# Kernel optimization log

Hardware: AMD Instinct MI355X
Metric: run time of the kernel (lower is better)

Reference implementation:

```python
import jax, jax.numpy as jnp
import numpy as np

B, N, DIN, DM, NH = 8, 2048, 256, 256, 4
DK = DM // NH


def setup_inputs() -> dict:
    key = jax.random.key(0)
    ks = jax.random.split(key, 8)
    x = jax.random.normal(ks[0], (B, N, DIN), dtype=jnp.float32)
    # contiguous valid ranges per sample (padding on both ends), matching
    # the module's assumption that torch.where(mask)[0][0]/[−1] define a span
    starts = jax.random.randint(ks[1], (B,), 0, N // 8)
    lens = jax.random.randint(ks[2], (B,), N // 2, N - N // 8)
    pos = jnp.arange(N)
    attention_mask = ((pos[None, :] >= starts[:, None])
                      & (pos[None, :] < starts[:, None] + lens[:, None])).astype(jnp.int32)
    s = 0.02
    Wq = jax.random.normal(ks[3], (DIN, DM), jnp.float32) * s
    Wk = jax.random.normal(ks[4], (DIN, DM), jnp.float32) * s
    Wv = jax.random.normal(ks[5], (DIN, DM), jnp.float32) * s
    Wo = jax.random.normal(ks[6], (DM, DM), jnp.float32) * s
    bq = jnp.zeros((DM,), jnp.float32)
    bk = jnp.zeros((DM,), jnp.float32)
    bv = jnp.zeros((DM,), jnp.float32)
    bo = jnp.zeros((DM,), jnp.float32)
    return {"x": x, "attention_mask": attention_mask,
            "Wq": Wq, "bq": bq, "Wk": Wk, "bk": bk,
            "Wv": Wv, "bv": bv, "Wo": Wo, "bo": bo}


def reference(x, attention_mask, Wq, bq, Wk, bk, Wv, bv, Wo, bo):
    b, n, _ = x.shape
    nh, dk = NH, DK
    scale = 1.0 / np.sqrt(dk)
    q = (x @ Wq + bq).reshape(b, n, nh, dk).transpose(0, 2, 1, 3)  # [b,h,n,dk]
    k = (x @ Wk + bk).reshape(b, n, nh, dk).transpose(0, 2, 1, 3)
    v = (x @ Wv + bv).reshape(b, n, nh, dk).transpose(0, 2, 1, 3)
    dist = jnp.einsum('bhid,bhjd->bhij', q, k) * scale  # [b,h,n,n]

    # Vectorized equivalent of the per-sample python-loop mask:
    # start = first True index; end = last True index (torch slice start:end
    # is EXCLUSIVE of the last valid position -- preserved faithfully).
    m = attention_mask.astype(bool)
    pos = jnp.arange(n)
    start = jnp.argmax(m, axis=1)                      # [b]
    end = n - 1 - jnp.argmax(m[:, ::-1], axis=1)       # [b] last True index
    valid = (pos[None, :] >= start[:, None]) & (pos[None, :] < end[:, None])  # [b,n]
    bias = jnp.where(valid[:, :, None] & valid[:, None, :], 0.0, -1e10)       # [b,n,n]

    dist = jax.nn.softmax(dist + bias[:, None, :, :], axis=-1)
    att = jnp.einsum('bhij,bhjd->bhid', dist, v)       # [b,h,n,dk]
    att = att.transpose(0, 2, 1, 3).reshape(b, n, nh * dk)
    return att @ Wo + bo
```

## Files before the change

### kernel.cpp

```cpp
#include <hip/hip_runtime.h>
#include <hip/hip_bf16.h>
#include <math.h>

namespace {
constexpr int Bb  = 8;
constexpr int Nn  = 2048;
constexpr int DIN_ = 256;
constexpr int DM_  = 256;
constexpr int NH_  = 4;
constexpr int DK_  = 64;
constexpr int BH_  = Bb * NH_;
constexpr float SCALE = 0.125f;
}

typedef __attribute__((ext_vector_type(8))) _Float16 half8;
typedef __attribute__((ext_vector_type(2))) __fp16 fp16x2;
typedef __attribute__((ext_vector_type(4))) float f32x4;

static __device__ __forceinline__ unsigned pkrtz_u32(float a, float b) {
    union { fp16x2 h; unsigned u; } u;
    u.h = __builtin_amdgcn_cvt_pkrtz(a, b);
    return u.u;
}

static __device__ __forceinline__ half8 h8_from_u32x4(unsigned w0, unsigned w1,
                                                      unsigned w2, unsigned w3) {
    union { unsigned u[4]; half8 h; } u;
    u.u[0] = w0; u.u[1] = w1; u.u[2] = w2; u.u[3] = w3;
    return u.h;
}

__global__ __launch_bounds__(256) void prep_kernel(
    const int* __restrict__ mask, int* __restrict__ bounds,
    const float* __restrict__ x, _Float16* __restrict__ xh,
    const float* __restrict__ W0, const float* __restrict__ W1,
    const float* __restrict__ W2, const float* __restrict__ W3,
    _Float16* __restrict__ T0, _Float16* __restrict__ T1,
    _Float16* __restrict__ T2, _Float16* __restrict__ T3)
{
    const int bid = blockIdx.x;
    const int tid = threadIdx.x;
    if (bid < 8) {
        const int b = bid;
        __shared__ int smin[256], smax[256];
        int lmin = Nn, lmax = -1;
        for (int i = tid; i < Nn; i += 256) {
            if (mask[b * Nn + i]) {
                if (i < lmin) lmin = i;
                if (i > lmax) lmax = i;
            }
        }
        smin[tid] = lmin; smax[tid] = lmax;
        __syncthreads();
        for (int s = 128; s > 0; s >>= 1) {
            if (tid < s) {
                smin[tid] = min(smin[tid], smin[tid + s]);
                smax[tid] = max(smax[tid], smax[tid + s]);
            }
            __syncthreads();
        }
        if (tid == 0) { bounds[b * 2] = smin[0]; bounds[b * 2 + 1] = smax[0]; }
    } else if (bid < 8 + 2048) {
        const size_t i = ((size_t)(bid - 8) * 256 + tid) * 8;
        float4 v0 = *(const float4*)&x[i];
        float4 v1 = *(const float4*)&x[i + 4];
        _Float16 h[8];
        h[0]=(_Float16)v0.x; h[1]=(_Float16)v0.y; h[2]=(_Float16)v0.z; h[3]=(_Float16)v0.w;
        h[4]=(_Float16)v1.x; h[5]=(_Float16)v1.y; h[6]=(_Float16)v1.z; h[7]=(_Float16)v1.w;
        *(uint4*)&xh[i] = *(const uint4*)h;
    } else {
        const int lin = bid - 2056;
        const int wsel = lin >> 6;
        const float* W; _Float16* T;
        switch (wsel) {
            case 0: W = W0; T = T0; break;
            case 1: W = W1; T = T1; break;
            case 2: W = W2; T = T2; break;
            default: W = W3; T = T3; break;
        }
        const int idx = (lin & 63) * 256 + tid;
        const int n = idx & 255;
        const int k0 = (idx >> 8) << 2;
        _Float16 h4[4];
        #pragma unroll
        for (int j = 0; j < 4; ++j) h4[j] = (_Float16)W[(size_t)(k0 + j) * 256 + n];
        *(uint2*)&T[(size_t)n * 256 + k0] = *(const uint2*)h4;
    }
}

__global__ __launch_bounds__(256) void qkv_mfma(
    const _Float16* __restrict__ xh,
    const _Float16* __restrict__ Wtq, const float* __restrict__ bq,
    const _Float16* __restrict__ Wtk, const float* __restrict__ bk,
    const _Float16* __restrict__ Wtv, const float* __restrict__ bv,
    _Float16* __restrict__ Qh, _Float16* __restrict__ Kh, _Float16* __restrict__ Vt)
{
    const int z = blockIdx.z;
    const _Float16* Wt; const float* bias;
    if (z == 0)      { Wt = Wtq; bias = bq; }
    else if (z == 1) { Wt = Wtk; bias = bk; }
    else             { Wt = Wtv; bias = bv; }

    const int m0 = blockIdx.x * 128;
    const int n0 = blockIdx.y * 64;
    const int tid = threadIdx.x;
    const int w = tid >> 6, lane = tid & 63;
    const int a = lane & 15, g = lane >> 4;
    const int mb = m0 + 32 * w;

    f32x4 d0[4] = {{0,0,0,0},{0,0,0,0},{0,0,0,0},{0,0,0,0}};
    f32x4 d1[4] = {{0,0,0,0},{0,0,0,0},{0,0,0,0},{0,0,0,0}};

    const _Float16* A0 = xh + (size_t)(mb + a) * 256 + 8 * g;
    const _Float16* A1 = xh + (size_t)(mb + 16 + a) * 256 + 8 * g;
    const _Float16* Wr0 = Wt + (size_t)(n0 +  0 + a) * 256 + 8 * g;
    const _Float16* Wr1 = Wt + (size_t)(n0 + 16 + a) * 256 + 8 * g;
    const _Float16* Wr2 = Wt + (size_t)(n0 + 32 + a) * 256 + 8 * g;
    const _Float16* Wr3 = Wt + (size_t)(n0 + 48 + a) * 256 + 8 * g;

    #pragma unroll
    for (int kc = 0; kc < 8; ++kc) {
        const half8 af0 = *(const half8*)(A0 + 32 * kc);
        const half8 af1 = *(const half8*)(A1 + 32 * kc);
        const half8 b0 = *(const half8*)(Wr0 + 32 * kc);
        const half8 b1 = *(const half8*)(Wr1 + 32 * kc);
        const half8 b2 = *(const half8*)(Wr2 + 32 * kc);
        const half8 b3 = *(const half8*)(Wr3 + 32 * kc);
        d0[0] = __builtin_amdgcn_mfma_f32_16x16x32_f16(af0, b0, d0[0], 0,0,0);
        d1[0] = __builtin_amdgcn_mfma_f32_16x16x32_f16(af1, b0, d1[0], 0,0,0);
        d0[1] = __builtin_amdgcn_mfma_f32_16x16x32_f16(af0, b1, d0[1], 0,0,0);
        d1[1] = __builtin_amdgcn_mfma_f32_16x16x32_f16(af1, b1, d1[1], 0,0,0);
        d0[2] = __builtin_amdgcn_mfma_f32_16x16x32_f16(af0, b2, d0[2], 0,0,0);
        d1[2] = __builtin_amdgcn_mfma_f32_16x16x32_f16(af1, b2, d1[2], 0,0,0);
        d0[3] = __builtin_amdgcn_mfma_f32_16x16x32_f16(af0, b3, d0[3], 0,0,0);
        d1[3] = __builtin_amdgcn_mfma_f32_16x16x32_f16(af1, b3, d1[3], 0,0,0);
    }

    #pragma unroll
    for (int t = 0; t < 2; ++t) {
        const int mrow = mb + 16 * t + 4 * g;
        #pragma unroll
        for (int nf = 0; nf < 4; ++nf) {
            const f32x4 dv = t == 0 ? d0[nf] : d1[nf];
            const int n = n0 + 16 * nf + a;
            const float bs = bias[n];
            const int bh = (mrow >> 11) * NH_ + (n >> 6);
            const int dk = n & 63;
            if (z < 2) {
                _Float16* out = z ? Kh : Qh;
                #pragma unroll
                for (int r = 0; r < 4; ++r) {
                    const int tok = (mrow + r) & 2047;
                    out[((size_t)bh * Nn + tok) * DK_ + dk] = (_Float16)(dv[r] + bs);
                }
            } else {
                const int tok = mrow & 2047;
                uint2 pk;
                pk.x = pkrtz_u32(dv[0] + bs, dv[1] + bs);
                pk.y = pkrtz_u32(dv[2] + bs, dv[3] + bs);
                *(uint2*)&Vt[((size_t)bh * DK_ + dk) * Nn + tok] = pk;
            }
        }
    }
}

__global__ __launch_bounds__(256) void colmean_kernel(const _Float16* __restrict__ Vt,
                                                      float* __restrict__ cm) {
    const int bh = blockIdx.x;
    const int t = threadIdx.x;
    const int d = t >> 2, part = t & 3;
    const _Float16* src = Vt + ((size_t)bh * DK_ + d) * Nn + part * 512;
    float s = 0.f;
    for (int i = 0; i < 512; i += 8) {
        half8 v = *(const half8*)(src + i);
        #pragma unroll
        for (int j = 0; j < 8; ++j) s += (float)v[j];
    }
    __shared__ float red[64][4];
    red[d][part] = s;
    __syncthreads();
    if (part == 0)
        cm[bh * DK_ + d] = (red[d][0] + red[d][1] + red[d][2] + red[d][3]) * (1.0f / 2048.0f);
}

__global__ __launch_bounds__(256) void flash_mfma(
    const _Float16* __restrict__ Q, const _Float16* __restrict__ K,
    const _Float16* __restrict__ Vt, const int* __restrict__ bounds,
    _Float16* __restrict__ Oh, float* __restrict__ lw)
{
    const int bid = blockIdx.x;
    const int xcd = bid & 7;
    const int rest = bid >> 3;
    const int qb  = rest & 31;
    const int j   = (rest >> 5) & 3;
    const int s   = rest >> 7;
    const int bh  = j * 8 + xcd;
    const int b  = bh >> 2, h = bh & 3;
    const int q0 = qb * 64;
    const int tid  = threadIdx.x;
    const int w    = tid >> 6;
    const int lane = tid & 63;
    const int a = lane & 15, g = lane >> 4;
    const int start = bounds[2 * b], endv = bounds[2 * b + 1];

    if (q0 + 63 < start || q0 >= endv) return;

    __shared__ __align__(16) _Float16 kfr[2][8][512];
    __shared__ __align__(16) _Float16 vfr[2][8][512];

    const _Float16* Qb = Q  + (size_t)bh * Nn * DK_;
    const _Float16* Kb = K  + (size_t)bh * Nn * DK_;
    const _Float16* Vb = Vt + (size_t)bh * DK_ * Nn;

    const int qrow = q0 + 16 * w + a;
    const half8 qf0 = *(const half8*)&Qb[(size_t)qrow * DK_ + 8 * g];
    const half8 qf1 = *(const half8*)&Qb[(size_t)qrow * DK_ + 32 + 8 * g];

    float l_i = 0.0f;
    f32x4 o0 = {0.f,0.f,0.f,0.f}, o1 = {0.f,0.f,0.f,0.f};
    f32x4 o2 = {0.f,0.f,0.f,0.f}, o3 = {0.f,0.f,0.f,0.f};

#define STAGE(cbuf, kt_) do {                                                        \
        _Pragma("unroll")                                                            \
        for (int ff = 0; ff < 2; ++ff) {                                             \
            const int f  = 2 * w + ff;                                               \
            const int tt = f >> 1, cc = f & 1;                                       \
            const _Float16* ks = &Kb[(size_t)((kt_) + 16 * tt + a) * DK_ + 32 * cc + 8 * g]; \
            __builtin_amdgcn_global_load_lds(                                        \
                (const __attribute__((address_space(1))) void*)ks,                   \
                (__attribute__((address_space(3))) void*)&kfr[cbuf][f][0], 16, 0, 0);\
            const _Float16* vs = &Vb[(size_t)(16 * tt + a) * Nn + (kt_) + 32 * cc + 8 * g]; \
            __builtin_amdgcn_global_load_lds(                                        \
                (const __attribute__((address_space(1))) void*)vs,                   \
                (__attribute__((address_space(3))) void*)&vfr[cbuf][f][0], 16, 0, 0);\
        }                                                                            \
    } while (0)

    const int t0 = start >> 6, t1 = (endv + 63) >> 6;
    const int nt = t1 - t0;
    const int n0t = (nt + 1) >> 1;
    const int ts = (s == 0) ? t0 : t0 + n0t;
    const int te = (s == 0) ? t0 + n0t : t1;

    if (ts < te) {
        const int lo = ts * 64, hiend = te * 64;
        int c = 0;
        STAGE(0, lo);

        for (int kt = lo; kt < hiend; kt += 64) {
            const int nxt = kt + 64;
            if (nxt < hiend) {
                STAGE(c ^ 1, nxt);
                asm volatile("s_waitcnt vmcnt(4)" ::: "memory");
            } else {
                asm volatile("s_waitcnt vmcnt(0)" ::: "memory");
            }
            __builtin_amdgcn_s_barrier();

            const _Float16* kf = &kfr[c][0][0];
            const _Float16* vf = &vfr[c][0][0];

            f32x4 st0 = {0.f,0.f,0.f,0.f}, st1 = {0.f,0.f,0.f,0.f};
            f32x4 st2 = {0.f,0.f,0.f,0.f}, st3 = {0.f,0.f,0.f,0.f};
            st0 = __builtin_amdgcn_mfma_f32_16x16x32_f16(*(const half8*)&kf[0*512 + lane*8], qf0, st0, 0,0,0);
            st0 = __builtin_amdgcn_mfma_f32_16x16x32_f16(*(const half8*)&kf[1*512 + lane*8], qf1, st0, 0,0,0);
            st1 = __builtin_amdgcn_mfma_f32_16x16x32_f16(*(const half8*)&kf[2*512 + lane*8], qf0, st1, 0,0,0);
            st1 = __builtin_amdgcn_mfma_f32_16x16x32_f16(*(const half8*)&kf[3*512 + lane*8], qf1, st1, 0,0,0);
            st2 = __builtin_amdgcn_mfma_f32_16x16x32_f16(*(const half8*)&kf[4*512 + lane*8], qf0, st2, 0,0,0);
            st2 = __builtin_amdgcn_mfma_f32_16x16x32_f16(*(const half8*)&kf[5*512 + lane*8], qf1, st2, 0,0,0);
            st3 = __builtin_amdgcn_mfma_f32_16x16x32_f16(*(const half8*)&kf[6*512 + lane*8], qf0, st3, 0,0,0);
            st3 = __builtin_amdgcn_mfma_f32_16x16x32_f16(*(const half8*)&kf[7*512 + lane*8], qf1, st3, 0,0,0);

            float pv[4][4];
            float rsum = 0.0f;
            const bool edge = (kt < start) || (kt + 64 > endv);
            if (edge) {
                #pragma unroll
                for (int t = 0; t < 4; ++t) {
                    const f32x4 sv = (t == 0) ? st0 : (t == 1) ? st1 : (t == 2) ? st2 : st3;
                    #pragma unroll
                    for (int r = 0; r < 4; ++r) {
                        const int col = kt + 16 * t + 4 * g + r;
                        const bool ok = (col >= start) && (col < endv);
                        const float e = ok ? __expf(sv[r] * SCALE) : 0.0f;
                        pv[t][r] = e;
                        rsum += e;
                    }
                }
            } else {
                #pragma unroll
                for (int t = 0; t < 4; ++t) {
                    const f32x4 sv = (t == 0) ? st0 : (t == 1) ? st1 : (t == 2) ? st2 : st3;
                    #pragma unroll
                    for (int r = 0; r < 4; ++r) {
                        const float e = __expf(sv[r] * SCALE);
                        pv[t][r] = e;
                        rsum += e;
                    }
                }
            }
            rsum += __shfl_xor(rsum, 16, 64);
            rsum += __shfl_xor(rsum, 32, 64);
            l_i += rsum;

            unsigned pk[4][2];
            #pragma unroll
            for (int t = 0; t < 4; ++t) {
                pk[t][0] = pkrtz_u32(pv[t][0], pv[t][1]);
                pk[t][1] = pkrtz_u32(pv[t][2], pv[t][3]);
            }
            const int gsel = g >> 1;
            unsigned aw[2][4];
            #pragma unroll
            for (int cq = 0; cq < 2; ++cq) {
                #pragma unroll
                for (int wd = 0; wd < 4; ++wd) {
                    const int srcLane = a + 16 * (2 * (g & 1) + (wd >> 1));
                    const int lo2 = __shfl((int)pk[2 * cq    ][wd & 1], srcLane, 64);
                    const int hi2 = __shfl((int)pk[2 * cq + 1][wd & 1], srcLane, 64);
                    aw[cq][wd] = (unsigned)(gsel ? hi2 : lo2);
                }
            }
            const half8 pa0 = h8_from_u32x4(aw[0][0], aw[0][1], aw[0][2], aw[0][3]);
            const half8 pa1 = h8_from_u32x4(aw[1][0], aw[1][1], aw[1][2], aw[1][3]);

            o0 = __builtin_amdgcn_mfma_f32_16x16x32_f16(pa0, *(const half8*)&vf[0*512 + lane*8], o0, 0,0,0);
            o0 = __builtin_amdgcn_mfma_f32_16x16x32_f16(pa1, *(const half8*)&vf[1*512 + lane*8], o0, 0,0,0);
            o1 = __builtin_amdgcn_mfma_f32_16x16x32_f16(pa0, *(const half8*)&vf[2*512 + lane*8], o1, 0,0,0);
            o1 = __builtin_amdgcn_mfma_f32_16x16x32_f16(pa1, *(const half8*)&vf[3*512 + lane*8], o1, 0,0,0);
            o2 = __builtin_amdgcn_mfma_f32_16x16x32_f16(pa0, *(const half8*)&vf[4*512 + lane*8], o2, 0,0,0);
            o2 = __builtin_amdgcn_mfma_f32_16x16x32_f16(pa1, *(const half8*)&vf[5*512 + lane*8], o2, 0,0,0);
            o3 = __builtin_amdgcn_mfma_f32_16x16x32_f16(pa0, *(const half8*)&vf[6*512 + lane*8], o3, 0,0,0);
            o3 = __builtin_amdgcn_mfma_f32_16x16x32_f16(pa1, *(const half8*)&vf[7*512 + lane*8], o3, 0,0,0);

            asm volatile("" ::: "memory");
            __builtin_amdgcn_s_barrier();
            c ^= 1;
        }
    }
#undef STAGE

    const size_t half = (size_t)Bb * Nn * DM_;
    _Float16* ob = Oh + (size_t)s * half + ((size_t)b * Nn) * DM_ + h * DK_;
    #pragma unroll
    for (int td = 0; td < 4; ++td) {
        const f32x4 ov = (td == 0) ? o0 : (td == 1) ? o1 : (td == 2) ? o2 : o3;
        #pragma unroll
        for (int r = 0; r < 4; ++r) {
            const int qr = q0 + 16 * w + 4 * g + r;
            ob[(size_t)qr * DM_ + 16 * td + a] = (_Float16)ov[r];
        }
    }
    if (g == 0) {
        const int tok = q0 + 16 * w + a;
        lw[(size_t)s * BH_ * Nn + (size_t)bh * Nn + tok] = l_i;
    }
}

__global__ __launch_bounds__(256) void combine_kernel(
    const _Float16* __restrict__ Oh, const float* __restrict__ lw,
    const int* __restrict__ bounds, const float* __restrict__ cm,
    _Float16* __restrict__ att)
{
    const int b  = blockIdx.y;
    const int q0 = blockIdx.x * 64;
    const int t  = threadIdx.x;
    const int row = q0 + (t >> 2);
    const int h   = t & 3;
    const int c0  = h * 64;
    const int start = bounds[2 * b], endv = bounds[2 * b + 1];
    const bool valid = (row >= start) && (row < endv);

    const size_t half = (size_t)Bb * Nn * DM_;
    const size_t rowoff = ((size_t)b * Nn + row) * DM_ + c0;

    float inv = 0.0f;
    if (valid) {
        const int bh = b * NH_ + h;
        const float l0 = lw[(size_t)bh * Nn + row];
        const float l1 = lw[(size_t)BH_ * Nn + (size_t)bh * Nn + row];
        inv = 1.0f / (l0 + l1);
    }

    #pragma unroll
    for (int jj = 0; jj < 64; jj += 8) {
        _Float16 o[8];
        if (valid) {
            half8 a0 = *(const half8*)&Oh[rowoff + jj];
            half8 a1 = *(const half8*)&Oh[half + rowoff + jj];
            #pragma unroll
            for (int k = 0; k < 8; ++k)
                o[k] = (_Float16)(((float)a0[k] + (float)a1[k]) * inv);
        } else {
            #pragma unroll
            for (int k = 0; k < 8; ++k)
                o[k] = (_Float16)cm[b * DM_ + c0 + jj + k];
        }
        *(uint4*)&att[rowoff + jj] = *(const uint4*)o;
    }
}

__global__ __launch_bounds__(256) void proj_mfma(
    const _Float16* __restrict__ A, const _Float16* __restrict__ Wt,
    const float* __restrict__ bias, float* __restrict__ out)
{
    const int m0 = blockIdx.x * 128;
    const int n0 = blockIdx.y * 64;
    const int tid = threadIdx.x;
    const int w = tid >> 6, lane = tid & 63;
    const int a = lane & 15, g = lane >> 4;
    const int mb = m0 + 32 * w;

    f32x4 d0[4] = {{0,0,0,0},{0,0,0,0},{0,0,0,0},{0,0,0,0}};
    f32x4 d1[4] = {{0,0,0,0},{0,0,0,0},{0,0,0,0},{0,0,0,0}};

    const _Float16* A0 = A + (size_t)(mb + a) * 256 + 8 * g;
    const _Float16* A1 = A + (size_t)(mb + 16 + a) * 256 + 8 * g;
    const _Float16* Wr0 = Wt + (size_t)(n0 +  0 + a) * 256 + 8 * g;
    const _Float16* Wr1 = Wt + (size_t)(n0 + 16 + a) * 256 + 8 * g;
    const _Float16* Wr2 = Wt + (size_t)(n0 + 32 + a) * 256 + 8 * g;
    const _Float16* Wr3 = Wt + (size_t)(n0 + 48 + a) * 256 + 8 * g;

    #pragma unroll
    for (int kc = 0; kc < 8; ++kc) {
        const half8 af0 = *(const half8*)(A0 + 32 * kc);
        const half8 af1 = *(const half8*)(A1 + 32 * kc);
        const half8 b0 = *(const half8*)(Wr0 + 32 * kc);
        const half8 b1 = *(const half8*)(Wr1 + 32 * kc);
        const half8 b2 = *(const half8*)(Wr2 + 32 * kc);
        const half8 b3 = *(const half8*)(Wr3 + 32 * kc);
        d0[0] = __builtin_amdgcn_mfma_f32_16x16x32_f16(af0, b0, d0[0], 0,0,0);
        d1[0] = __builtin_amdgcn_mfma_f32_16x16x32_f16(af1, b0, d1[0], 0,0,0);
        d0[1] = __builtin_amdgcn_mfma_f32_16x16x32_f16(af0, b1, d0[1], 0,0,0);
        d1[1] = __builtin_amdgcn_mfma_f32_16x16x32_f16(af1, b1, d1[1], 0,0,0);
        d0[2] = __builtin_amdgcn_mfma_f32_16x16x32_f16(af0, b2, d0[2], 0,0,0);
        d1[2] = __builtin_amdgcn_mfma_f32_16x16x32_f16(af1, b2, d1[2], 0,0,0);
        d0[3] = __builtin_amdgcn_mfma_f32_16x16x32_f16(af0, b3, d0[3], 0,0,0);
        d1[3] = __builtin_amdgcn_mfma_f32_16x16x32_f16(af1, b3, d1[3], 0,0,0);
    }

    #pragma unroll
    for (int t = 0; t < 2; ++t) {
        const int mrow = mb + 16 * t + 4 * g;
        #pragma unroll
        for (int nf = 0; nf < 4; ++nf) {
            const f32x4 dv = t == 0 ? d0[nf] : d1[nf];
            const int n = n0 + 16 * nf + a;
            const float bs = bias[n];
            #pragma unroll
            for (int r = 0; r < 4; ++r)
                out[(size_t)(mrow + r) * DM_ + n] = dv[r] + bs;
        }
    }
}

extern "C" void kernel_launch(void* const* d_in, const int* in_sizes, int n_in,
                              void* d_out, int out_size, void* d_ws, size_t ws_size,
                              hipStream_t stream)
{
    const float* x    = (const float*)d_in[0];
    const int*   mask = (const int*)d_in[1];
    const float* Wq   = (const float*)d_in[2];
    const float* bq   = (const float*)d_in[3];
    const float* Wk   = (const float*)d_in[4];
    const float* bk   = (const float*)d_in[5];
    const float* Wv   = (const float*)d_in[6];
    const float* bv   = (const float*)d_in[7];
    const float* Wo   = (const float*)d_in[8];
    const float* bo   = (const float*)d_in[9];
    float* out = (float*)d_out;

    char* ws = (char*)d_ws;
    size_t off = 0;
    int* bounds = (int*)ws;                 off += 256;
    float* cmv  = (float*)(ws + off);       off += (size_t)BH_ * DK_ * sizeof(float);
    off = (off + 255) & ~(size_t)255;
    float* lw   = (float*)(ws + off);       off += (size_t)2 * BH_ * Nn * sizeof(float);
    const size_t h16_bytes = (size_t)BH_ * Nn * DK_ * sizeof(_Float16);
    _Float16* xh  = (_Float16*)(ws + off); off += h16_bytes;
    _Float16* Qh  = (_Float16*)(ws + off); off += h16_bytes;
    _Float16* Kh  = (_Float16*)(ws + off); off += h16_bytes;
    _Float16* Vt  = (_Float16*)(ws + off); off += h16_bytes;
    _Float16* Oh  = (_Float16*)(ws + off); off += 2 * h16_bytes;
    _Float16* ath = (_Float16*)(ws + off); off += h16_bytes;
    _Float16* Wtq = (_Float16*)(ws + off); off += 256 * 256 * sizeof(_Float16);
    _Float16* Wtk = (_Float16*)(ws + off); off += 256 * 256 * sizeof(_Float16);
    _Float16* Wtv = (_Float16*)(ws + off); off += 256 * 256 * sizeof(_Float16);
    _Float16* Wto = (_Float16*)(ws + off); off += 256 * 256 * sizeof(_Float16);

    prep_kernel<<<2312, 256, 0, stream>>>(mask, bounds, x, xh,
                                          Wq, Wk, Wv, Wo, Wtq, Wtk, Wtv, Wto);

    dim3 g1(Bb * Nn / 128, DM_ / 64, 3);
    qkv_mfma<<<g1, 256, 0, stream>>>(xh, Wtq, bq, Wtk, bk, Wtv, bv, Qh, Kh, Vt);

    colmean_kernel<<<BH_, 256, 0, stream>>>(Vt, cmv);

    flash_mfma<<<2048, 256, 0, stream>>>(Qh, Kh, Vt, bounds, Oh, lw);

    dim3 gc(Nn / 64, Bb);
    combine_kernel<<<gc, 256, 0, stream>>>(Oh, lw, bounds, cmv, ath);

    dim3 g3(Bb * Nn / 128, DM_ / 64);
    proj_mfma<<<g3, 256, 0, stream>>>(ath, Wto, bo, out);
}
```

Baseline: 208.3 us.

## Fuse x fp16 conversion into QKV GEMM, LDS-tile GEMMs, add MFMA priority hints

Drops the separate x-to-fp16 pass in the prep kernel. The QKV GEMM now reads fp32 x directly, converts it while staging into swizzled LDS tiles, and loads weights with global_load_lds. The output projection GEMM gets the same LDS tiling, and the Q/K epilogue is transposed so it writes 4 packed halves per store. The flash kernel wraps its MFMA blocks in s_setprio hints. This removes an intermediate buffer round trip and scattered global fragment loads, at the cost of extra LDS barriers and each QKV block re-converting x.

```diff
diff --git a/kernel.cpp b/kernel.cpp
--- a/kernel.cpp
+++ b/kernel.cpp
@@ -32,7 +32,6 @@
 
 __global__ __launch_bounds__(256) void prep_kernel(
     const int* __restrict__ mask, int* __restrict__ bounds,
-    const float* __restrict__ x, _Float16* __restrict__ xh,
     const float* __restrict__ W0, const float* __restrict__ W1,
     const float* __restrict__ W2, const float* __restrict__ W3,
     _Float16* __restrict__ T0, _Float16* __restrict__ T1,
@@ -60,16 +59,8 @@
             __syncthreads();
         }
         if (tid == 0) { bounds[b * 2] = smin[0]; bounds[b * 2 + 1] = smax[0]; }
-    } else if (bid < 8 + 2048) {
-        const size_t i = ((size_t)(bid - 8) * 256 + tid) * 8;
-        float4 v0 = *(const float4*)&x[i];
-        float4 v1 = *(const float4*)&x[i + 4];
-        _Float16 h[8];
-        h[0]=(_Float16)v0.x; h[1]=(_Float16)v0.y; h[2]=(_Float16)v0.z; h[3]=(_Float16)v0.w;
-        h[4]=(_Float16)v1.x; h[5]=(_Float16)v1.y; h[6]=(_Float16)v1.z; h[7]=(_Float16)v1.w;
-        *(uint4*)&xh[i] = *(const uint4*)h;
     } else {
-        const int lin = bid - 2056;
+        const int lin = bid - 8;
         const int wsel = lin >> 6;
         const float* W; _Float16* T;
         switch (wsel) {
@@ -89,76 +80,125 @@
 }
 
 __global__ __launch_bounds__(256) void qkv_mfma(
-    const _Float16* __restrict__ xh,
+    const float* __restrict__ x,
     const _Float16* __restrict__ Wtq, const float* __restrict__ bq,
     const _Float16* __restrict__ Wtk, const float* __restrict__ bk,
     const _Float16* __restrict__ Wtv, const float* __restrict__ bv,
     _Float16* __restrict__ Qh, _Float16* __restrict__ Kh, _Float16* __restrict__ Vt)
 {
-    const int z = blockIdx.z;
+    const int zsel = blockIdx.y >> 2;
+    const int n0 = (blockIdx.y & 3) * 64;
+    const int m0 = blockIdx.x * 128;
     const _Float16* Wt; const float* bias;
-    if (z == 0)      { Wt = Wtq; bias = bq; }
-    else if (z == 1) { Wt = Wtk; bias = bk; }
-    else             { Wt = Wtv; bias = bv; }
-
-    const int m0 = blockIdx.x * 128;
-    const int n0 = blockIdx.y * 64;
+    if (zsel == 0)      { Wt = Wtq; bias = bq; }
+    else if (zsel == 1) { Wt = Wtk; bias = bk; }
+    else                { Wt = Wtv; bias = bv; }
+
     const int tid = threadIdx.x;
     const int w = tid >> 6, lane = tid & 63;
     const int a = lane & 15, g = lane >> 4;
-    const int mb = m0 + 32 * w;
-
-    f32x4 d0[4] = {{0,0,0,0},{0,0,0,0},{0,0,0,0},{0,0,0,0}};
-    f32x4 d1[4] = {{0,0,0,0},{0,0,0,0},{0,0,0,0},{0,0,0,0}};
-
-    const _Float16* A0 = xh + (size_t)(mb + a) * 256 + 8 * g;
-    const _Float16* A1 = xh + (size_t)(mb + 16 + a) * 256 + 8 * g;
-    const _Float16* Wr0 = Wt + (size_t)(n0 +  0 + a) * 256 + 8 * g;
-    const _Float16* Wr1 = Wt + (size_t)(n0 + 16 + a) * 256 + 8 * g;
-    const _Float16* Wr2 = Wt + (size_t)(n0 + 32 + a) * 256 + 8 * g;
-    const _Float16* Wr3 = Wt + (size_t)(n0 + 48 + a) * 256 + 8 * g;
-
-    #pragma unroll
-    for (int kc = 0; kc < 8; ++kc) {
-        const half8 af0 = *(const half8*)(A0 + 32 * kc);
-        const half8 af1 = *(const half8*)(A1 + 32 * kc);
-        const half8 b0 = *(const half8*)(Wr0 + 32 * kc);
-        const half8 b1 = *(const half8*)(Wr1 + 32 * kc);
-        const half8 b2 = *(const half8*)(Wr2 + 32 * kc);
-        const half8 b3 = *(const half8*)(Wr3 + 32 * kc);
-        d0[0] = __builtin_amdgcn_mfma_f32_16x16x32_f16(af0, b0, d0[0], 0,0,0);
-        d1[0] = __builtin_amdgcn_mfma_f32_16x16x32_f16(af1, b0, d1[0], 0,0,0);
-        d0[1] = __builtin_amdgcn_mfma_f32_16x16x32_f16(af0, b1, d0[1], 0,0,0);
-        d1[1] = __builtin_amdgcn_mfma_f32_16x16x32_f16(af1, b1, d1[1], 0,0,0);
-        d0[2] = __builtin_amdgcn_mfma_f32_16x16x32_f16(af0, b2, d0[2], 0,0,0);
-        d1[2] = __builtin_amdgcn_mfma_f32_16x16x32_f16(af1, b2, d1[2], 0,0,0);
-        d0[3] = __builtin_amdgcn_mfma_f32_16x16x32_f16(af0, b3, d0[3], 0,0,0);
-        d1[3] = __builtin_amdgcn_mfma_f32_16x16x32_f16(af1, b3, d1[3], 0,0,0);
-    }
-
-    #pragma unroll
-    for (int t = 0; t < 2; ++t) {
-        const int mrow = mb + 16 * t + 4 * g;
+    const int b = m0 >> 11;
+
+    __shared__ __align__(16) _Float16 As[128 * 64];
+    __shared__ __align__(16) _Float16 Bs[64 * 64];
+
+    f32x4 acc[4][2] = {{{0,0,0,0},{0,0,0,0}},{{0,0,0,0},{0,0,0,0}},
+                       {{0,0,0,0},{0,0,0,0}},{{0,0,0,0},{0,0,0,0}}};
+
+    for (int step = 0; step < 4; ++step) {
+        const int k0 = step * 64;
+        {
+            const int rb = tid >> 3, fc = tid & 7;
+            #pragma unroll
+            for (int p = 0; p < 4; ++p) {
+                const int row = p * 32 + rb;
+                const float4 v0 = *(const float4*)&x[(size_t)(m0 + row) * 256 + k0 + fc * 8];
+                const float4 v1 = *(const float4*)&x[(size_t)(m0 + row) * 256 + k0 + fc * 8 + 4];
+                _Float16 h[8];
+                h[0]=(_Float16)v0.x; h[1]=(_Float16)v0.y; h[2]=(_Float16)v0.z; h[3]=(_Float16)v0.w;
+                h[4]=(_Float16)v1.x; h[5]=(_Float16)v1.y; h[6]=(_Float16)v1.z; h[7]=(_Float16)v1.w;
+                const int byo = (fc * 16) ^ ((row & 7) << 4);
+                *(uint4*)((char*)As + row * 128 + byo) = *(const uint4*)h;
+            }
+        }
+        #pragma unroll
+        for (int i = 0; i < 2; ++i) {
+            const int f = 2 * w + i;
+            const int rowl = f * 8 + (lane >> 3);
+            const int byo = ((lane & 7) * 16) ^ ((rowl & 7) << 4);
+            const char* src = (const char*)(Wt + (size_t)(n0 + rowl) * 256 + k0) + byo;
+            __builtin_amdgcn_global_load_lds(
+                (const __attribute__((address_space(1))) void*)src,
+                (__attribute__((address_space(3))) void*)((char*)Bs + f * 1024), 16, 0, 0);
+        }
+        __syncthreads();
+
+        #pragma unroll
+        for (int kc = 0; kc < 2; ++kc) {
+            half8 xf[2], wf[4];
+            #pragma unroll
+            for (int tt = 0; tt < 2; ++tt) {
+                const int row = 32 * w + 16 * tt + a;
+                const int byo = (kc * 64 + g * 16) ^ ((row & 7) << 4);
+                xf[tt] = *(const half8*)((const char*)As + row * 128 + byo);
+            }
+            #pragma unroll
+            for (int nf = 0; nf < 4; ++nf) {
+                const int row = 16 * nf + a;
+                const int byo = (kc * 64 + g * 16) ^ ((row & 7) << 4);
+                wf[nf] = *(const half8*)((const char*)Bs + row * 128 + byo);
+            }
+            if (zsel < 2) {
+                #pragma unroll
+                for (int nf = 0; nf < 4; ++nf)
+                    #pragma unroll
+                    for (int tt = 0; tt < 2; ++tt)
+                        acc[nf][tt] = __builtin_amdgcn_mfma_f32_16x16x32_f16(wf[nf], xf[tt], acc[nf][tt], 0,0,0);
+            } else {
+                #pragma unroll
+                for (int nf = 0; nf < 4; ++nf)
+                    #pragma unroll
+                    for (int tt = 0; tt < 2; ++tt)
+                        acc[nf][tt] = __builtin_amdgcn_mfma_f32_16x16x32_f16(xf[tt], wf[nf], acc[nf][tt], 0,0,0);
+            }
+        }
+        __syncthreads();
+    }
+
+    if (zsel < 2) {
+        _Float16* out = zsel ? Kh : Qh;
         #pragma unroll
         for (int nf = 0; nf < 4; ++nf) {
-            const f32x4 dv = t == 0 ? d0[nf] : d1[nf];
+            const int nb = n0 + 16 * nf + 4 * g;
+            const f32x4 bi = *(const f32x4*)&bias[nb];
+            const int h = nb >> 6, dkb = nb & 63;
+            #pragma unroll
+            for (int tt = 0; tt < 2; ++tt) {
+                const int tok = (m0 + 32 * w + 16 * tt + a) & 2047;
+                const f32x4 d = acc[nf][tt];
+                _Float16 q4[4];
+                q4[0] = (_Float16)(d[0] + bi[0]);
+                q4[1] = (_Float16)(d[1] + bi[1]);
+                q4[2] = (_Float16)(d[2] + bi[2]);
+                q4[3] = (_Float16)(d[3] + bi[3]);
+                *(uint2*)&out[(((size_t)(b * NH_ + h)) * Nn + tok) * DK_ + dkb] = *(const uint2*)q4;
+            }
+        }
+    } else {
+        const int h = n0 >> 6;
+        #pragma unroll
+        for (int nf = 0; nf < 4; ++nf) {
             const int n = n0 + 16 * nf + a;
             const float bs = bias[n];
-            const int bh = (mrow >> 11) * NH_ + (n >> 6);
-            const int dk = n & 63;
-            if (z < 2) {
-                _Float16* out = z ? Kh : Qh;
-                #pragma unroll
-                for (int r = 0; r < 4; ++r) {
-                    const int tok = (mrow + r) & 2047;
-                    out[((size_t)bh * Nn + tok) * DK_ + dk] = (_Float16)(dv[r] + bs);
-                }
-            } else {
-                const int tok = mrow & 2047;
+            const int dk = 16 * nf + a;
+            #pragma unroll
+            for (int tt = 0; tt < 2; ++tt) {
+                const int tokb = (m0 + 32 * w + 16 * tt + 4 * g) & 2047;
+                const f32x4 d = acc[nf][tt];
                 uint2 pk;
-                pk.x = pkrtz_u32(dv[0] + bs, dv[1] + bs);
-                pk.y = pkrtz_u32(dv[2] + bs, dv[3] + bs);
-                *(uint2*)&Vt[((size_t)bh * DK_ + dk) * Nn + tok] = pk;
+                pk.x = pkrtz_u32(d[0] + bs, d[1] + bs);
+                pk.y = pkrtz_u32(d[2] + bs, d[3] + bs);
+                *(uint2*)&Vt[(((size_t)(b * NH_ + h)) * DK_ + dk) * Nn + tokb] = pk;
             }
         }
     }
@@ -262,6 +302,7 @@
 
             f32x4 st0 = {0.f,0.f,0.f,0.f}, st1 = {0.f,0.f,0.f,0.f};
             f32x4 st2 = {0.f,0.f,0.f,0.f}, st3 = {0.f,0.f,0.f,0.f};
+            __builtin_amdgcn_s_setprio(1);
             st0 = __builtin_amdgcn_mfma_f32_16x16x32_f16(*(const half8*)&kf[0*512 + lane*8], qf0, st0, 0,0,0);
             st0 = __builtin_amdgcn_mfma_f32_16x16x32_f16(*(const half8*)&kf[1*512 + lane*8], qf1, st0, 0,0,0);
             st1 = __builtin_amdgcn_mfma_f32_16x16x32_f16(*(const half8*)&kf[2*512 + lane*8], qf0, st1, 0,0,0);
@@ -270,6 +311,7 @@
             st2 = __builtin_amdgcn_mfma_f32_16x16x32_f16(*(const half8*)&kf[5*512 + lane*8], qf1, st2, 0,0,0);
             st3 = __builtin_amdgcn_mfma_f32_16x16x32_f16(*(const half8*)&kf[6*512 + lane*8], qf0, st3, 0,0,0);
             st3 = __builtin_amdgcn_mfma_f32_16x16x32_f16(*(const half8*)&kf[7*512 + lane*8], qf1, st3, 0,0,0);
+            __builtin_amdgcn_s_setprio(0);
 
             float pv[4][4];
             float rsum = 0.0f;
@@ -324,6 +366,7 @@
             const half8 pa0 = h8_from_u32x4(aw[0][0], aw[0][1], aw[0][2], aw[0][3]);
             const half8 pa1 = h8_from_u32x4(aw[1][0], aw[1][1], aw[1][2], aw[1][3]);
 
+            __builtin_amdgcn_s_setprio(1);
             o0 = __builtin_amdgcn_mfma_f32_16x16x32_f16(pa0, *(const half8*)&vf[0*512 + lane*8], o0, 0,0,0);
             o0 = __builtin_amdgcn_mfma_f32_16x16x32_f16(pa1, *(const half8*)&vf[1*512 + lane*8], o0, 0,0,0);
             o1 = __builtin_amdgcn_mfma_f32_16x16x32_f16(pa0, *(const half8*)&vf[2*512 + lane*8], o1, 0,0,0);
@@ -332,6 +375,7 @@
             o2 = __builtin_amdgcn_mfma_f32_16x16x32_f16(pa1, *(const half8*)&vf[5*512 + lane*8], o2, 0,0,0);
             o3 = __builtin_amdgcn_mfma_f32_16x16x32_f16(pa0, *(const half8*)&vf[6*512 + lane*8], o3, 0,0,0);
             o3 = __builtin_amdgcn_mfma_f32_16x16x32_f16(pa1, *(const half8*)&vf[7*512 + lane*8], o3, 0,0,0);
+            __builtin_amdgcn_s_setprio(0);
 
             asm volatile("" ::: "memory");
             __builtin_amdgcn_s_barrier();
@@ -409,47 +453,72 @@
     const int tid = threadIdx.x;
     const int w = tid >> 6, lane = tid & 63;
     const int a = lane & 15, g = lane >> 4;
-    const int mb = m0 + 32 * w;
-
-    f32x4 d0[4] = {{0,0,0,0},{0,0,0,0},{0,0,0,0},{0,0,0,0}};
-    f32x4 d1[4] = {{0,0,0,0},{0,0,0,0},{0,0,0,0},{0,0,0,0}};
-
-    const _Float16* A0 = A + (size_t)(mb + a) * 256 + 8 * g;
-    const _Float16* A1 = A + (size_t)(mb + 16 + a) * 256 + 8 * g;
-    const _Float16* Wr0 = Wt + (size_t)(n0 +  0 + a) * 256 + 8 * g;
-    const _Float16* Wr1 = Wt + (size_t)(n0 + 16 + a) * 256 + 8 * g;
-    const _Float16* Wr2 = Wt + (size_t)(n0 + 32 + a) * 256 + 8 * g;
-    const _Float16* Wr3 = Wt + (size_t)(n0 + 48 + a) * 256 + 8 * g;
+
+    __shared__ __align__(16) _Float16 As[128 * 64];
+    __shared__ __align__(16) _Float16 Bs[64 * 64];
+
+    f32x4 acc[2][4] = {{{0,0,0,0},{0,0,0,0},{0,0,0,0},{0,0,0,0}},
+                       {{0,0,0,0},{0,0,0,0},{0,0,0,0},{0,0,0,0}}};
+
+    for (int step = 0; step < 4; ++step) {
+        const int k0 = step * 64;
+        #pragma unroll
+        for (int i = 0; i < 4; ++i) {
+            const int f = 4 * w + i;
+            const int rowl = f * 8 + (lane >> 3);
+            const int byo = ((lane & 7) * 16) ^ ((rowl & 7) << 4);
+            const char* src = (const char*)(A + (size_t)(m0 + rowl) * 256 + k0) + byo;
+            __builtin_amdgcn_global_load_lds(
+                (const __attribute__((address_space(1))) void*)src,
+                (__attribute__((address_space(3))) void*)((char*)As + f * 1024), 16, 0, 0);
+        }
+        #pragma unroll
+        for (int i = 0; i < 2; ++i) {
+            const int f = 2 * w + i;
+            const int rowl = f * 8 + (lane >> 3);
+            const int byo = ((lane & 7) * 16) ^ ((rowl & 7) << 4);
+            const char* src = (const char*)(Wt + (size_t)(n0 + rowl) * 256 + k0) + byo;
+            __builtin_amdgcn_global_load_lds(
+                (const __attribute__((address_space(1))) void*)src,
+                (__attribute__((address_space(3))) void*)((char*)Bs + f * 1024), 16, 0, 0);
+        }
+        __syncthreads();
+
+        #pragma unroll
+        for (int kc = 0; kc < 2; ++kc) {
+            half8 af[2], wf[4];
+            #pragma unroll
+            for (int tt = 0; tt < 2; ++tt) {
+                const int row = 32 * w + 16 * tt + a;
+                const int byo = (kc * 64 + g * 16) ^ ((row & 7) << 4);
+                af[tt] = *(const half8*)((const char*)As + row * 128 + byo);
+            }
+            #pragma unroll
+            for (int nf = 0; nf < 4; ++nf) {
+                const int row = 16 * nf + a;
+                const int byo = (kc * 64 + g * 16) ^ ((row & 7) << 4);
+                wf[nf] = *(const half8*)((const char*)Bs + row * 128 + byo);
+            }
+            #pragma unroll
+            for (int tt = 0; tt < 2; ++tt)
+                #pragma unroll
+                for (int nf = 0; nf < 4; ++nf)
+                    acc[tt][nf] = __builtin_amdgcn_mfma_f32_16x16x32_f16(af[tt], wf[nf], acc[tt][nf], 0,0,0);
+        }
+        __syncthreads();
+    }
 
     #pragma unroll
-    for (int kc = 0; kc < 8; ++kc) {
-        const half8 af0 = *(const half8*)(A0 + 32 * kc);
-        const half8 af1 = *(const half8*)(A1 + 32 * kc);
-        const half8 b0 = *(const half8*)(Wr0 + 32 * kc);
-        const half8 b1 = *(const half8*)(Wr1 + 32 * kc);
-        const half8 b2 = *(const half8*)(Wr2 + 32 * kc);
-        const half8 b3 = *(const half8*)(Wr3 + 32 * kc);
-        d0[0] = __builtin_amdgcn_mfma_f32_16x16x32_f16(af0, b0, d0[0], 0,0,0);
-        d1[0] = __builtin_amdgcn_mfma_f32_16x16x32_f16(af1, b0, d1[0], 0,0,0);
-        d0[1] = __builtin_amdgcn_mfma_f32_16x16x32_f16(af0, b1, d0[1], 0,0,0);
-        d1[1] = __builtin_amdgcn_mfma_f32_16x16x32_f16(af1, b1, d1[1], 0,0,0);
-        d0[2] = __builtin_amdgcn_mfma_f32_16x16x32_f16(af0, b2, d0[2], 0,0,0);
-        d1[2] = __builtin_amdgcn_mfma_f32_16x16x32_f16(af1, b2, d1[2], 0,0,0);
-        d0[3] = __builtin_amdgcn_mfma_f32_16x16x32_f16(af0, b3, d0[3], 0,0,0);
-        d1[3] = __builtin_amdgcn_mfma_f32_16x16x32_f16(af1, b3, d1[3], 0,0,0);
-    }
-
-    #pragma unroll
-    for (int t = 0; t < 2; ++t) {
-        const int mrow = mb + 16 * t + 4 * g;
+    for (int tt = 0; tt < 2; ++tt) {
         #pragma unroll
         for (int nf = 0; nf < 4; ++nf) {
-            const f32x4 dv = t == 0 ? d0[nf] : d1[nf];
             const int n = n0 + 16 * nf + a;
             const float bs = bias[n];
+            const f32x4 d = acc[tt][nf];
+            const int mrow = m0 + 32 * w + 16 * tt + 4 * g;
             #pragma unroll
             for (int r = 0; r < 4; ++r)
-                out[(size_t)(mrow + r) * DM_ + n] = dv[r] + bs;
+                out[(size_t)(mrow + r) * 256 + n] = d[r] + bs;
         }
     }
 }
@@ -477,7 +546,6 @@
     off = (off + 255) & ~(size_t)255;
     float* lw   = (float*)(ws + off);       off += (size_t)2 * BH_ * Nn * sizeof(float);
     const size_t h16_bytes = (size_t)BH_ * Nn * DK_ * sizeof(_Float16);
-    _Float16* xh  = (_Float16*)(ws + off); off += h16_bytes;
     _Float16* Qh  = (_Float16*)(ws + off); off += h16_bytes;
     _Float16* Kh  = (_Float16*)(ws + off); off += h16_bytes;
     _Float16* Vt  = (_Float16*)(ws + off); off += h16_bytes;
@@ -488,11 +556,11 @@
     _Float16* Wtv = (_Float16*)(ws + off); off += 256 * 256 * sizeof(_Float16);
     _Float16* Wto = (_Float16*)(ws + off); off += 256 * 256 * sizeof(_Float16);
 
-    prep_kernel<<<2312, 256, 0, stream>>>(mask, bounds, x, xh,
-                                          Wq, Wk, Wv, Wo, Wtq, Wtk, Wtv, Wto);
-
-    dim3 g1(Bb * Nn / 128, DM_ / 64, 3);
-    qkv_mfma<<<g1, 256, 0, stream>>>(xh, Wtq, bq, Wtk, bk, Wtv, bv, Qh, Kh, Vt);
+    prep_kernel<<<264, 256, 0, stream>>>(mask, bounds, Wq, Wk, Wv, Wo,
+                                         Wtq, Wtk, Wtv, Wto);
+
+    dim3 g1(128, 12);
+    qkv_mfma<<<g1, 256, 0, stream>>>(x, Wtq, bq, Wtk, bk, Wtv, bv, Qh, Kh, Vt);
 
     colmean_kernel<<<BH_, 256, 0, stream>>>(Vt, cmv);
 
@@ -501,6 +569,6 @@
     dim3 gc(Nn / 64, Bb);
     combine_kernel<<<gc, 256, 0, stream>>>(Oh, lw, bounds, cmv, ath);
 
-    dim3 g3(Bb * Nn / 128, DM_ / 64);
+    dim3 g3(128, 4);
     proj_mfma<<<g3, 256, 0, stream>>>(ath, Wto, bo, out);
 }
```

After: 183.9 us. 11.7% less time.
